# Kernel optimization log

Measured on AMD Instinct MI355X. Metric: run time of the kernel, lower is better.

Reference implementation:

```python
import jax, jax.numpy as jnp
import numpy as np

# Water box constants: n_atoms=192 -> 64 oxygens (type 8) + 128 hydrogens (type 1)
N_O, N_H = 64, 128
XLIM = 6.0  # params.max_rdf_dist


def _hist(d, bins):
    """np.histogram-equivalent fixed-bin histogram of 1-D values d."""
    nb = bins.shape[0] - 1
    idx = jnp.clip(jnp.searchsorted(bins, d, side='right') - 1, 0, nb - 1)
    w = ((d >= bins[0]) & (d <= bins[-1])).astype(jnp.float32)
    return jnp.zeros((nb,), jnp.float32).at[idx].add(w)


def _pair_rdf(wrapped, idx0, idx1, lattices, bins):
    # wrapped: [T, N, 3]; replicates distance_pbc_select + histogram/RDF math
    x0 = wrapped[:, idx0]                       # [T, n0, 3] (type1 atoms)
    x1 = wrapped[:, idx1]                       # [T, n1, 3] (type2 atoms)
    # x0.repeat([1,n1,1]) vs x1.repeat_interleave(n0) == outer pairing (x1 outer, x0 inner)
    delta = jnp.abs(x0[:, None, :, :] - x1[:, :, None, :])   # [T, n1, n0, 3]
    delta = jnp.where(delta > 0.5 * lattices, delta - lattices, delta)
    s = (delta ** 2).sum(-1)                    # [T, n1, n0]
    # safe sqrt (self-pairs give exact zeros)
    d = jnp.where(s > 0, jnp.sqrt(jnp.where(s > 0, s, 1.0)), 0.0)
    T = d.shape[0]
    P = d.shape[1] * d.shape[2]
    d = d.reshape(T, P)
    hists = jax.vmap(lambda dd: _hist(dd, bins))(d)          # [T, nb]
    vol = jnp.prod(lattices)
    shell = (4.0 / 3.0) * jnp.pi * (bins[1:] ** 3 - bins[:-1] ** 3)
    # aggregate RDF over all frames (zeros fall below bins[0]=1e-6, excluded)
    Z1 = (T * P / vol) * shell
    data_rdf = hists.sum(0) / Z1
    # per-frame RDFs, renormalized to the aggregate RDF's total mass
    Z2 = (T / vol) * shell
    rdfs = hists / Z2
    rdfs = rdfs / rdfs.sum(1, keepdims=True) * data_rdf.sum()
    return rdfs.mean(0)                          # [nb]


def setup_inputs() -> dict:
    key = jax.random.key(0)
    k0, k1, k2, k3 = jax.random.split(key, 4)
    T, R, N, nb = 100, 8, 192, 600
    stacked_radii = jax.random.normal(k0, (T, R, N, 3), jnp.float32) * 5.0
    ptypes = jnp.tile(jnp.array([8, 1, 1], jnp.int32), N // 3)  # O,H,H per water
    lattices = jnp.full((3,), 12.42, jnp.float32)
    bins = jnp.asarray(np.linspace(1e-6, XLIM, nb + 1), jnp.float32)
    gt_oo = jax.random.uniform(k1, (1, nb), jnp.float32)
    gt_hh = jax.random.uniform(k2, (1, nb), jnp.float32)
    gt_ho = jax.random.uniform(k3, (1, nb), jnp.float32)
    return dict(stacked_radii=stacked_radii, ptypes=ptypes, lattices=lattices,
                bins=bins, gt_oo=gt_oo, gt_hh=gt_hh, gt_ho=gt_ho)


def reference(stacked_radii, ptypes, lattices, bins, gt_oo, gt_hh, gt_ho):
    idx_O = jnp.nonzero(ptypes == 8, size=N_O)[0]
    idx_H = jnp.nonzero(ptypes == 1, size=N_H)[0]

    def per_replica(data):                       # data: [T, N, 3]
        wrapped = data / lattices % 1 * lattices  # PBC wrap into box
        rdf_oo = _pair_rdf(wrapped, idx_O, idx_O, lattices, bins)
        rdf_hh = _pair_rdf(wrapped, idx_H, idx_H, lattices, bins)
        rdf_ho = _pair_rdf(wrapped, idx_H, idx_O, lattices, bins)
        maes = jnp.stack([
            XLIM * jnp.abs(rdf_oo[None] - gt_oo).mean(),
            XLIM * jnp.abs(rdf_hh[None] - gt_hh).mean(),
            XLIM * jnp.abs(rdf_ho[None] - gt_ho).mean(),
        ])
        return jnp.concatenate([rdf_oo, rdf_hh, rdf_ho]), maes.max()

    # [T, R, N, 3] -> [R, T, N, 3], vmap over replicas
    rdf_list, max_maes = jax.vmap(per_replica)(jnp.swapaxes(stacked_radii, 0, 1))
    return rdf_list, max_maes
```

## Files before the change

kernel.cpp:

```cpp
#include <hip/hip_runtime.h>

#define T_STEPS 100
#define R_REP   8
#define NBINS   600
#define NCOPY   8

__global__ __launch_bounds__(256) void rdf_fused_kernel(
    const float* __restrict__ radii,
    const float* __restrict__ lattices,
    const float* __restrict__ bins,
    float* __restrict__ acc,
    float* __restrict__ sigsum)
{
#pragma clang fp contract(off)
    __shared__ float    Tq[NBINS + 2];
    __shared__ unsigned hist3[3][4][NBINS];
    __shared__ float4   sH[128];
    __shared__ float4   sO[64];
    __shared__ float    sredw[4][3];
    __shared__ float    sInv[3];

    const int blk = blockIdx.x;
    const int r   = blk % R_REP;
    const int tid = threadIdx.x;
    const int wid = tid >> 6;
    const int lane = tid & 63;

    for (int b = tid; b <= NBINS + 1; b += 256) {
        if (b <= NBINS) {
            float e = bins[b];
            unsigned u = __float_as_uint(e * e);
            while (sqrtf(__uint_as_float(u)) <  e) ++u;
            while (sqrtf(__uint_as_float(u - 1)) >= e) --u;
            Tq[b] = __uint_as_float(u);
        } else {
            unsigned u = __float_as_uint(36.0f);
            while (sqrtf(__uint_as_float(u)) <= 6.0f) ++u;
            while (sqrtf(__uint_as_float(u - 1)) > 6.0f) --u;
            Tq[NBINS + 1] = __uint_as_float(u);
        }
    }
    {
        uint4* z = (uint4*)&hist3[0][0][0];
        for (int k = tid; k < 1800; k += 256) z[k] = make_uint4(0u, 0u, 0u, 0u);
    }

    const float L0 = lattices[0], L1 = lattices[1], L2 = lattices[2];
    const float* base = radii + (size_t)blk * 576;

    if (tid < 192) {
        int isH  = (tid >= 64);
        int a    = isH ? (tid - 64) : tid;
        int atom = isH ? (3 * (a >> 1) + 1 + (a & 1)) : (3 * a);
        const float* src = base + atom * 3;
        float x = src[0], y = src[1], z = src[2];
        float qx = x / L0; float wx = (qx - floorf(qx)) * L0;
        float qy = y / L1; float wy = (qy - floorf(qy)) * L1;
        float qz = z / L2; float wz = (qz - floorf(qz)) * L2;
        float4 w4 = make_float4(wx, wy, wz, 0.0f);
        if (isH) sH[a] = w4; else sO[a] = w4;
    }
    __syncthreads();

    const float T0 = Tq[0];
    const float TG = Tq[NBINS + 1];
    const float b0f = bins[0];
    const float invstep = (float)NBINS / (6.0f - b0f);

    auto bin_pair = [&](unsigned* myh, float4 A, float4 B, unsigned w) {
#pragma clang fp contract(off)
        float dx = fabsf(A.x - B.x); dx = fminf(dx, fabsf(dx - L0));
        float dy = fabsf(A.y - B.y); dy = fminf(dy, fabsf(dy - L1));
        float dz = fabsf(A.z - B.z); dz = fminf(dz, fabsf(dz - L2));
        float s = dx * dx + dy * dy + dz * dz;
        if (s < T0 || s >= TG) return;
        float dhat = __builtin_amdgcn_sqrtf(s);
        int k0 = (int)((dhat - b0f) * invstep);
        if (k0 > NBINS - 1) k0 = NBINS - 1;
        float lo = Tq[k0], hi = Tq[k0 + 1];
        int bi = k0 + (int)(s >= hi) - (int)(s < lo);
        if (bi > NBINS - 1) bi = NBINS - 1;
        atomicAdd(&myh[bi], w);
    };

    {
        int i = tid & 63;
        int kbase = (tid >> 6) + 1;
        float4 A = sO[i];
#pragma unroll
        for (int it = 0; it < 8; ++it) {
            int k = kbase + it * 4;
            bin_pair(hist3[0][wid], A, sO[(i + k) & 63], (k == 32) ? 1u : 2u);
        }
    }
    {
        int i = tid & 127;
        int kbase = (tid >> 7) + 1;
        float4 A = sH[i];
#pragma unroll
        for (int it = 0; it < 32; ++it) {
            int k = kbase + it * 2;
            bin_pair(hist3[1][wid], A, sH[(i + k) & 127], (k == 64) ? 1u : 2u);
        }
        int jb = tid >> 7;
#pragma unroll
        for (int it = 0; it < 32; ++it)
            bin_pair(hist3[2][wid], A, sO[jb + it * 2], 1u);
    }
    __syncthreads();

    float fcs[3][3];
    float lsig0 = 0.0f, lsig1 = 0.0f, lsig2 = 0.0f;
#pragma unroll
    for (int ii = 0; ii < 3; ++ii) {
        int b = tid + ii * 256;
        if (b < NBINS) {
            float e0 = bins[b], e1 = bins[b + 1];
            float shell = 4.18879020478639053f * (e1 * e1 * e1 - e0 * e0 * e0);
            float is = 1.0f / shell;
            float f0 = (float)(hist3[0][0][b] + hist3[0][1][b] + hist3[0][2][b] + hist3[0][3][b]);
            float f1 = (float)(hist3[1][0][b] + hist3[1][1][b] + hist3[1][2][b] + hist3[1][3][b]);
            float f2 = (float)(hist3[2][0][b] + hist3[2][1][b] + hist3[2][2][b] + hist3[2][3][b]);
            fcs[ii][0] = f0; fcs[ii][1] = f1; fcs[ii][2] = f2;
            lsig0 += f0 * is; lsig1 += f1 * is; lsig2 += f2 * is;
        } else {
            fcs[ii][0] = 0.0f; fcs[ii][1] = 0.0f; fcs[ii][2] = 0.0f;
        }
    }
#pragma unroll
    for (int off = 32; off > 0; off >>= 1) {
        lsig0 += __shfl_down(lsig0, off, 64);
        lsig1 += __shfl_down(lsig1, off, 64);
        lsig2 += __shfl_down(lsig2, off, 64);
    }
    if (lane == 0) {
        sredw[wid][0] = lsig0; sredw[wid][1] = lsig1; sredw[wid][2] = lsig2;
    }
    __syncthreads();
    if (tid < 3) {
        float sg = sredw[0][tid] + sredw[1][tid] + sredw[2][tid] + sredw[3][tid];
        sInv[tid] = 1.0f / sg;
        atomicAdd(&sigsum[r * 3 + tid], sg);
    }
    __syncthreads();

    const float i0 = sInv[0], i1 = sInv[1], i2 = sInv[2];
    float* accr = acc + ((size_t)(blk & (NCOPY - 1)) * 24 + (size_t)r * 3) * NBINS;
#pragma unroll
    for (int ii = 0; ii < 3; ++ii) {
        int b = tid + ii * 256;
        if (b < NBINS) {
            float f0 = fcs[ii][0], f1 = fcs[ii][1], f2 = fcs[ii][2];
            if (f0 != 0.0f) atomicAdd(&accr[0 * NBINS + b], f0 * i0);
            if (f1 != 0.0f) atomicAdd(&accr[1 * NBINS + b], f1 * i1);
            if (f2 != 0.0f) atomicAdd(&accr[2 * NBINS + b], f2 * i2);
        }
    }
}

__global__ __launch_bounds__(640) void rdf_final_kernel(
    const float* __restrict__ acc,
    const float* __restrict__ sigsum,
    const float* __restrict__ bins,
    const float* __restrict__ lattices,
    const float* __restrict__ gt_oo,
    const float* __restrict__ gt_hh,
    const float* __restrict__ gt_ho,
    float* __restrict__ out)
{
#pragma clang fp contract(off)
    __shared__ float sred[640];

    const int blk = blockIdx.x;
    const int p = blk % 3, r = blk / 3;
    const int tid = threadIdx.x;

    const float vol = lattices[0] * lattices[1] * lattices[2];
    const float Pf  = (p == 0) ? 4096.0f : ((p == 1) ? 16384.0f : 8192.0f);
    const float S   = vol / ((float)T_STEPS * Pf) * sigsum[blk];

    const float* gt = (p == 0) ? gt_oo : ((p == 1) ? gt_hh : gt_ho);
    float lacc = 0.0f;
    if (tid < NBINS) {
        float a = 0.0f;
#pragma unroll
        for (int c = 0; c < NCOPY; ++c)
            a += acc[(c * 24 + blk) * NBINS + tid];
        float e0 = bins[tid], e1 = bins[tid + 1];
        float shell = 4.18879020478639053f * (e1 * e1 * e1 - e0 * e0 * e0);
        float v = S * (1.0f / (float)T_STEPS) * (1.0f / shell) * a;
        out[r * 1800 + p * 600 + tid] = v;
        lacc = fabsf(v - gt[tid]);
    }
    sred[tid] = lacc;
    __syncthreads();
    for (int s2 = 512; s2 > 0; s2 >>= 1) {
        if (tid < s2 && tid + s2 < 640) sred[tid] += sred[tid + s2];
        __syncthreads();
    }
    if (tid == 0) {
        float mae = 6.0f * (sred[0] / 600.0f);
        atomicMax((int*)&out[14400 + r], __float_as_int(mae));
    }
}

extern "C" void kernel_launch(void* const* d_in, const int* in_sizes, int n_in,
                              void* d_out, int out_size, void* d_ws, size_t ws_size,
                              hipStream_t stream) {
    const float* radii    = (const float*)d_in[0];
    const float* lattices = (const float*)d_in[2];
    const float* bins     = (const float*)d_in[3];
    const float* gt_oo    = (const float*)d_in[4];
    const float* gt_hh    = (const float*)d_in[5];
    const float* gt_ho    = (const float*)d_in[6];
    float* out = (float*)d_out;

    float* acc    = (float*)d_ws;
    float* sigsum = acc + NCOPY * 24 * NBINS;

    hipMemsetAsync(d_ws, 0, (NCOPY * 24 * NBINS + 24) * sizeof(float), stream);

    hipLaunchKernelGGL(rdf_fused_kernel, dim3(T_STEPS * R_REP), dim3(256), 0, stream,
                       radii, lattices, bins, acc, sigsum);
    hipLaunchKernelGGL(rdf_final_kernel, dim3(24), dim3(640), 0, stream,
                       acc, sigsum, bins, lattices, gt_oo, gt_hh, gt_ho, out);
}
```

Baseline: 107.6 us.

## Split RDF histogram work into one block per pair type and frame

The fused kernel that computed all three pair-type histograms in one block per frame/replica is split so each block handles a single pair type. This triples the grid size and cuts per-block shared memory from three histogram sets to one, which could raise occupancy and parallelism. In exchange, each block repeats the bin-threshold table setup and the atom loads, and the blocks become unbalanced: HH and HO blocks do 4x the pair work of OO blocks. It also adds more global atomics into the accumulation copies.

```diff
diff --git a/kernel.cpp b/kernel.cpp
--- a/kernel.cpp
+++ b/kernel.cpp
@@ -5,7 +5,7 @@
 #define NBINS   600
 #define NCOPY   8
 
-__global__ __launch_bounds__(256) void rdf_fused_kernel(
+__global__ __launch_bounds__(256) void rdf_hist_kernel(
     const float* __restrict__ radii,
     const float* __restrict__ lattices,
     const float* __restrict__ bins,
@@ -14,14 +14,16 @@
 {
 #pragma clang fp contract(off)
     __shared__ float    Tq[NBINS + 2];
-    __shared__ unsigned hist3[3][4][NBINS];
-    __shared__ float4   sH[128];
-    __shared__ float4   sO[64];
-    __shared__ float    sredw[4][3];
-    __shared__ float    sInv[3];
+    __shared__ unsigned shist[4][NBINS];
+    __shared__ float4   sA[128];
+    __shared__ float4   sB[64];
+    __shared__ float    sredw[4];
+    __shared__ float    sInvSig;
 
     const int blk = blockIdx.x;
-    const int r   = blk % R_REP;
+    const int p   = blk % 3;
+    const int t   = (blk / 3) % T_STEPS;
+    const int r   = blk / (3 * T_STEPS);
     const int tid = threadIdx.x;
     const int wid = tid >> 6;
     const int lane = tid & 63;
@@ -41,33 +43,38 @@
         }
     }
     {
-        uint4* z = (uint4*)&hist3[0][0][0];
-        for (int k = tid; k < 1800; k += 256) z[k] = make_uint4(0u, 0u, 0u, 0u);
+        uint4* z = (uint4*)&shist[0][0];
+        for (int k = tid; k < 600; k += 256) z[k] = make_uint4(0u, 0u, 0u, 0u);
     }
 
     const float L0 = lattices[0], L1 = lattices[1], L2 = lattices[2];
-    const float* base = radii + (size_t)blk * 576;
-
-    if (tid < 192) {
-        int isH  = (tid >= 64);
-        int a    = isH ? (tid - 64) : tid;
-        int atom = isH ? (3 * (a >> 1) + 1 + (a & 1)) : (3 * a);
-        const float* src = base + atom * 3;
-        float x = src[0], y = src[1], z = src[2];
-        float qx = x / L0; float wx = (qx - floorf(qx)) * L0;
-        float qy = y / L1; float wy = (qy - floorf(qy)) * L1;
-        float qz = z / L2; float wz = (qz - floorf(qz)) * L2;
-        float4 w4 = make_float4(wx, wy, wz, 0.0f);
-        if (isH) sH[a] = w4; else sO[a] = w4;
-    }
+    const float* base = radii + (size_t)(t * R_REP + r) * 576;
+
+    auto load_set = [&](float4* dst, int n, bool isH) {
+#pragma clang fp contract(off)
+        for (int a = tid; a < n; a += 256) {
+            int atom = isH ? (3 * (a >> 1) + 1 + (a & 1)) : (3 * a);
+            const float* src = base + atom * 3;
+            float x = src[0], y = src[1], z = src[2];
+            float qx = x / L0; float wx = (qx - floorf(qx)) * L0;
+            float qy = y / L1; float wy = (qy - floorf(qy)) * L1;
+            float qz = z / L2; float wz = (qz - floorf(qz)) * L2;
+            dst[a] = make_float4(wx, wy, wz, 0.0f);
+        }
+    };
+
+    if (p == 0)      { load_set(sA, 64, false); }
+    else if (p == 1) { load_set(sA, 128, true); }
+    else             { load_set(sA, 128, true); load_set(sB, 64, false); }
     __syncthreads();
 
     const float T0 = Tq[0];
     const float TG = Tq[NBINS + 1];
     const float b0f = bins[0];
     const float invstep = (float)NBINS / (6.0f - b0f);
-
-    auto bin_pair = [&](unsigned* myh, float4 A, float4 B, unsigned w) {
+    unsigned* myh = shist[wid];
+
+    auto bin_pair = [&](float4 A, float4 B, unsigned w) {
 #pragma clang fp contract(off)
         float dx = fabsf(A.x - B.x); dx = fminf(dx, fabsf(dx - L0));
         float dy = fabsf(A.y - B.y); dy = fminf(dy, fabsf(dy - L1));
@@ -83,78 +90,66 @@
         atomicAdd(&myh[bi], w);
     };
 
-    {
+    if (p == 2) {
+        float4 A = sA[tid & 127];
+        int jb = tid >> 7;
+#pragma unroll
+        for (int it = 0; it < 32; ++it)
+            bin_pair(A, sB[jb + it * 2], 1u);
+    } else if (p == 1) {
+        int i = tid & 127;
+        float4 A = sA[i];
+        int kbase = (tid >> 7) + 1;
+#pragma unroll
+        for (int it = 0; it < 32; ++it) {
+            int k = kbase + it * 2;
+            bin_pair(A, sA[(i + k) & 127], (k == 64) ? 1u : 2u);
+        }
+    } else {
         int i = tid & 63;
+        float4 A = sA[i];
         int kbase = (tid >> 6) + 1;
-        float4 A = sO[i];
 #pragma unroll
         for (int it = 0; it < 8; ++it) {
             int k = kbase + it * 4;
-            bin_pair(hist3[0][wid], A, sO[(i + k) & 63], (k == 32) ? 1u : 2u);
-        }
-    }
-    {
-        int i = tid & 127;
-        int kbase = (tid >> 7) + 1;
-        float4 A = sH[i];
-#pragma unroll
-        for (int it = 0; it < 32; ++it) {
-            int k = kbase + it * 2;
-            bin_pair(hist3[1][wid], A, sH[(i + k) & 127], (k == 64) ? 1u : 2u);
-        }
-        int jb = tid >> 7;
-#pragma unroll
-        for (int it = 0; it < 32; ++it)
-            bin_pair(hist3[2][wid], A, sO[jb + it * 2], 1u);
-    }
-    __syncthreads();
-
-    float fcs[3][3];
-    float lsig0 = 0.0f, lsig1 = 0.0f, lsig2 = 0.0f;
+            bin_pair(A, sA[(i + k) & 63], (k == 32) ? 1u : 2u);
+        }
+    }
+    __syncthreads();
+
+    float fcs[3];
+    float lsig = 0.0f;
 #pragma unroll
     for (int ii = 0; ii < 3; ++ii) {
         int b = tid + ii * 256;
         if (b < NBINS) {
             float e0 = bins[b], e1 = bins[b + 1];
             float shell = 4.18879020478639053f * (e1 * e1 * e1 - e0 * e0 * e0);
-            float is = 1.0f / shell;
-            float f0 = (float)(hist3[0][0][b] + hist3[0][1][b] + hist3[0][2][b] + hist3[0][3][b]);
-            float f1 = (float)(hist3[1][0][b] + hist3[1][1][b] + hist3[1][2][b] + hist3[1][3][b]);
-            float f2 = (float)(hist3[2][0][b] + hist3[2][1][b] + hist3[2][2][b] + hist3[2][3][b]);
-            fcs[ii][0] = f0; fcs[ii][1] = f1; fcs[ii][2] = f2;
-            lsig0 += f0 * is; lsig1 += f1 * is; lsig2 += f2 * is;
+            float f = (float)(shist[0][b] + shist[1][b] + shist[2][b] + shist[3][b]);
+            fcs[ii] = f;
+            lsig += f / shell;
         } else {
-            fcs[ii][0] = 0.0f; fcs[ii][1] = 0.0f; fcs[ii][2] = 0.0f;
-        }
-    }
-#pragma unroll
-    for (int off = 32; off > 0; off >>= 1) {
-        lsig0 += __shfl_down(lsig0, off, 64);
-        lsig1 += __shfl_down(lsig1, off, 64);
-        lsig2 += __shfl_down(lsig2, off, 64);
-    }
-    if (lane == 0) {
-        sredw[wid][0] = lsig0; sredw[wid][1] = lsig1; sredw[wid][2] = lsig2;
-    }
-    __syncthreads();
-    if (tid < 3) {
-        float sg = sredw[0][tid] + sredw[1][tid] + sredw[2][tid] + sredw[3][tid];
-        sInv[tid] = 1.0f / sg;
-        atomicAdd(&sigsum[r * 3 + tid], sg);
-    }
-    __syncthreads();
-
-    const float i0 = sInv[0], i1 = sInv[1], i2 = sInv[2];
-    float* accr = acc + ((size_t)(blk & (NCOPY - 1)) * 24 + (size_t)r * 3) * NBINS;
+            fcs[ii] = 0.0f;
+        }
+    }
+#pragma unroll
+    for (int off = 32; off > 0; off >>= 1) lsig += __shfl_down(lsig, off, 64);
+    if (lane == 0) sredw[wid] = lsig;
+    __syncthreads();
+    if (tid == 0) {
+        float sg = sredw[0] + sredw[1] + sredw[2] + sredw[3];
+        sInvSig = 1.0f / sg;
+        atomicAdd(&sigsum[r * 3 + p], sg);
+    }
+    __syncthreads();
+
+    const float isg = sInvSig;
+    float* accr = acc + ((size_t)(blk & (NCOPY - 1)) * 24 + (size_t)(r * 3 + p)) * NBINS;
 #pragma unroll
     for (int ii = 0; ii < 3; ++ii) {
         int b = tid + ii * 256;
-        if (b < NBINS) {
-            float f0 = fcs[ii][0], f1 = fcs[ii][1], f2 = fcs[ii][2];
-            if (f0 != 0.0f) atomicAdd(&accr[0 * NBINS + b], f0 * i0);
-            if (f1 != 0.0f) atomicAdd(&accr[1 * NBINS + b], f1 * i1);
-            if (f2 != 0.0f) atomicAdd(&accr[2 * NBINS + b], f2 * i2);
-        }
+        if (b < NBINS && fcs[ii] != 0.0f)
+            atomicAdd(&accr[b], fcs[ii] * isg);
     }
 }
 
@@ -220,7 +215,7 @@
 
     hipMemsetAsync(d_ws, 0, (NCOPY * 24 * NBINS + 24) * sizeof(float), stream);
 
-    hipLaunchKernelGGL(rdf_fused_kernel, dim3(T_STEPS * R_REP), dim3(256), 0, stream,
+    hipLaunchKernelGGL(rdf_hist_kernel, dim3(R_REP * T_STEPS * 3), dim3(256), 0, stream,
                        radii, lattices, bins, acc, sigsum);
     hipLaunchKernelGGL(rdf_final_kernel, dim3(24), dim3(640), 0, stream,
                        acc, sigsum, bins, lattices, gt_oo, gt_hh, gt_ho, out);
```

Measured after the change: 104.7 us. -2.8%, faster.
